# Kernel tuning notes

Measured on AMD Instinct MI355X. Metric: run time of the kernel, lower is better.

The kernel has to match this reference:

```python
import jax, jax.numpy as jnp
import numpy as np

BETA = 0.25  # commitment-loss weight (kwargs['beta'])


def setup_inputs() -> dict:
    key = jax.random.key(0)
    k1, k2 = jax.random.split(key)
    B, C, H, W = 16, 256, 64, 64
    K = 2048
    feats = jax.random.normal(k1, (B, C, H, W), dtype=jnp.float32)
    # nn.Embedding init: uniform(-1/n_codewords, 1/codeword_dim)
    codebook = jax.random.uniform(k2, (K, C), minval=-1.0 / K, maxval=1.0 / C,
                                  dtype=jnp.float32)
    return {"feats": feats, "codebook": codebook}


def reference(feats, codebook):
    B, C, H, W = feats.shape
    K = codebook.shape[0]
    z = jnp.transpose(feats, (0, 2, 3, 1))          # [B,H,W,C]
    zf = z.reshape(-1, C)                            # [N,C], N=B*H*W
    # squared-euclidean distances via ||z||^2 + ||e||^2 - 2 z.e : [N,K]
    d = (jnp.sum(zf * zf, axis=1, keepdims=True)
         + jnp.sum(codebook * codebook, axis=1)
         - 2.0 * (zf @ codebook.T))
    min_encoding_indices = jnp.argmin(d, axis=1)     # [N]
    mat_id_probs = jax.nn.softmax(-jnp.abs(d), axis=1)  # [N,K]
    z_q = codebook[min_encoding_indices].reshape(z.shape)  # [B,H,W,C]
    loss = (BETA * jnp.mean((jax.lax.stop_gradient(z_q) - z) ** 2)
            + jnp.mean((z_q - jax.lax.stop_gradient(z)) ** 2))
    # straight-through estimator
    z_q_st = z + jax.lax.stop_gradient(z_q - z)
    z_q_out = jnp.transpose(z_q_st, (0, 3, 1, 2))    # [B,C,H,W]
    idx_out = min_encoding_indices.reshape(B, H, W)
    probs_out = jnp.transpose(mat_id_probs.reshape(B, H, W, K), (0, 3, 1, 2))
    return z_q_out, idx_out, loss, probs_out
```

## Files before the change

kernel.cpp:

```cpp
#include <hip/hip_runtime.h>

#define HW 4096
#define CC 256
#define KK 2048
#define BB 16
#define NN (BB*HW)
#define RPB 128

#define ZQ_SZ   (BB*CC*HW)
#define IDX_OFF ZQ_SZ
#define LOSS_OFF (IDX_OFF + NN)
#define PROBS_OFF (LOSS_OFF + 1)

#define EH_OFF 0
#define EE_OFF 262144
#define EXT_OFF 264192
#define ZZ_OFF 280576

#define TAU 0.01f
#define CAND_CAP 512
#define KTC 32
#define KT_N 64
#define CS_N 17

typedef short bf16x8 __attribute__((ext_vector_type(8)));
typedef float f32x16 __attribute__((ext_vector_type(16)));
typedef unsigned int u32;

__device__ __forceinline__ void gload16(const void* g, void* l){
  __builtin_amdgcn_global_load_lds(
      (const __attribute__((address_space(1))) u32*)g,
      (__attribute__((address_space(3))) u32*)l, 16, 0, 0);
}

__device__ __forceinline__ unsigned short bf16rn(float x){
  unsigned u = __float_as_uint(x);
  return (unsigned short)((u + 0x7fffu + ((u >> 16) & 1u)) >> 16);
}

template<int STRIDE>
__device__ __forceinline__ float np_sumsq256(const float* __restrict__ a){
  float res0 = 0.f, res1 = 0.f;
  #pragma unroll
  for (int h = 0; h < 2; h++){
    const float* p = a + (size_t)h * 128 * STRIDE;
    float r[8];
    #pragma unroll
    for (int j = 0; j < 8; j++){ float x = p[(size_t)j * STRIDE]; r[j] = __fmul_rn(x, x); }
    for (int i = 8; i < 128; i += 8){
      #pragma unroll
      for (int j = 0; j < 8; j++){
        float x = p[(size_t)(i + j) * STRIDE];
        r[j] = __fadd_rn(r[j], __fmul_rn(x, x));
      }
    }
    float s = __fadd_rn(__fadd_rn(__fadd_rn(r[0], r[1]), __fadd_rn(r[2], r[3])),
                        __fadd_rn(__fadd_rn(r[4], r[5]), __fadd_rn(r[6], r[7])));
    if (h == 0) res0 = s; else res1 = s;
  }
  return __fadd_rn(res0, res1);
}

__global__ void k_prep2(const float* __restrict__ cb, float* __restrict__ out){
  const int k = blockIdx.x * 256 + threadIdx.x;
  unsigned short* eh = (unsigned short*)(out + EH_OFF);
  unsigned short* ex = (unsigned short*)(out + EXT_OFF);
  const float* row = cb + (size_t)k * CC;
  for (int c = 0; c < CC; c++) eh[k * CC + c] = bf16rn(row[c]);
  float ee = np_sumsq256<1>(row);
  out[EE_OFF + k] = ee;
  ex[k * 16] = bf16rn(-0.5f * ee);
  #pragma unroll
  for (int j = 1; j < 16; ++j) ex[k * 16 + j] = 0;
}

__global__ void k_zz(const float* __restrict__ feats, float* __restrict__ out){
  const int n = blockIdx.x * 256 + threadIdx.x;
  const int b = n >> 12, hw = n & 4095;
  out[ZZ_OFF + n] = np_sumsq256<HW>(feats + (size_t)b * CC * HW + hw);
}

__global__ __launch_bounds__(256, 4)
void k_mfma(const float* __restrict__ feats, const float* __restrict__ cb,
            float* __restrict__ out){
  __shared__ __align__(16) unsigned char lds_e[2][CS_N * 2 * KTC * 16];
  __shared__ unsigned long long rowkey[RPB];
  __shared__ int cand[CAND_CAP];
  __shared__ int cand_n;
  __shared__ float lsum;

  const int t = threadIdx.x;
  const int w = t >> 6, l = t & 63;
  const int grp = l >> 5;
  const int lane31 = l & 31;
  const int n0 = blockIdx.x * RPB;
  const int bi = n0 >> 12;
  const int hw0 = n0 & 4095;
  const int myhw = hw0 + w * 32 + lane31;

  if (t < RPB) rowkey[t] = ~0ull;
  if (t == 0){ cand_n = 0; lsum = 0.f; }

  bf16x8 ah0[16], ahx;
  {
    const float* zb = feats + (size_t)bi * CC * HW + myhw;
    #pragma unroll
    for (int cs = 0; cs < 16; ++cs){
      #pragma unroll
      for (int j = 0; j < 8; ++j)
        ah0[cs][j] = (short)bf16rn(zb[(size_t)(cs * 16 + grp * 8 + j) * HW]);
    }
    #pragma unroll
    for (int j = 0; j < 8; ++j) ahx[j] = 0;
    if (grp == 0) ahx[0] = (short)0x3F80;
  }

  const unsigned short* ehg = (const unsigned short*)(out + EH_OFF);
  const unsigned short* exg = (const unsigned short*)(out + EXT_OFF);

  int ofs_[4];
  #pragma unroll
  for (int i = 0; i < 4; ++i){
    int ix = i * 256 + t;
    int cd = ix & 31, g = (ix >> 5) & 1, cs = ix >> 6;
    ofs_[i] = cd * CC + cs * 16 + g * 8;
  }

#define STAGE(KT, B) { \
    const unsigned short* tb_ = ehg + (size_t)(KT) * (KTC * CC); \
    _Pragma("unroll") \
    for (int i_ = 0; i_ < 4; ++i_) \
      gload16(tb_ + ofs_[i_], &lds_e[B][(i_ * 256 + t) * 16]); \
    if (t < 64){ \
      int cd_ = t & 31, g_ = (t >> 5) & 1; \
      gload16(exg + ((size_t)((KT) * KTC + cd_) * 16 + g_ * 8), \
              &lds_e[B][(1024 + t) * 16]); \
    } }

#define COMPUTE(B) { \
    _Pragma("unroll") \
    for (int ii = 0; ii < 16; ++ii){ accA[ii] = 0.f; accB[ii] = 0.f; } \
    _Pragma("unroll") \
    for (int cs = 0; cs < 16; ++cs){ \
      const unsigned char* bp_ = &lds_e[B][(size_t)(cs * 2 + grp) * 512 + lane31 * 16]; \
      bf16x8 e_ = *(const bf16x8*)(bp_); \
      if (cs & 1) accB = __builtin_amdgcn_mfma_f32_32x32x16_bf16(e_, ah0[cs], accB, 0, 0, 0); \
      else        accA = __builtin_amdgcn_mfma_f32_32x32x16_bf16(e_, ah0[cs], accA, 0, 0, 0); \
    } \
    { \
      const unsigned char* bp_ = &lds_e[B][(size_t)(16 * 2 + grp) * 512 + lane31 * 16]; \
      bf16x8 e_ = *(const bf16x8*)(bp_); \
      accA = __builtin_amdgcn_mfma_f32_32x32x16_bf16(e_, ahx, accA, 0, 0, 0); \
    } }

  f32x16 accA, accB;
  float m0 = 3e38f, ss0 = 0.f, inv0 = 0.f;

  STAGE(0, 0);
  __syncthreads();

  for (int kt = 0; kt < 2 * KT_N; ++kt){
    const int tt = kt & 63;
    const int buf = kt & 1;
    if (kt < 2 * KT_N - 1) STAGE((kt + 1) & 63, buf ^ 1);
    COMPUTE(buf);
    if (kt < KT_N){
      #pragma unroll
      for (int r = 0; r < 16; ++r){
        float s = -2.f * (accA[r] + accB[r]);
        m0 = fminf(m0, s);
        ss0 += __expf(-s);
      }
      if (kt == KT_N - 1){
        m0 = fminf(m0, __shfl_xor(m0, 32));
        ss0 += __shfl_xor(ss0, 32);
        inv0 = 1.f / ss0;
      }
    } else {
      float* pb = out + (size_t)PROBS_OFF
                + (size_t)(bi * KK + tt * KTC + 4 * grp) * HW + myhw;
      #pragma unroll
      for (int r = 0; r < 16; ++r){
        int off = (r & 3) + 8 * (r >> 2);
        float s = -2.f * (accA[r] + accB[r]);
        pb[(size_t)off * HW] = __expf(-s) * inv0;
        if (s <= m0 + TAU){
          int sl = atomicAdd(&cand_n, 1);
          if (sl < CAND_CAP)
            cand[sl] = ((w * 32 + lane31) << 16) | (tt * KTC + 4 * grp + off);
        }
      }
    }
    __syncthreads();
  }

  int nc = cand_n; if (nc > CAND_CAP) nc = CAND_CAP;
  for (int i = t; i < nc; i += 256){
    int rc = cand[i];
    int rl = rc >> 16, code = rc & 0xffff;
    int n = n0 + rl;
    const float* zp = feats + (size_t)(n >> 12) * CC * HW + (n & 4095);
    const float* ep = cb + (size_t)code * CC;
    float a = 0.f;
    #pragma unroll 8
    for (int c = 0; c < CC; ++c) a = __builtin_fmaf(zp[(size_t)c * HW], ep[c], a);
    float t1 = __fadd_rn(out[ZZ_OFF + n], out[EE_OFF + code]);
    float d = __fadd_rn(t1, -2.f * a);
    unsigned long long key = ((unsigned long long)__float_as_uint(d) << 32) | (unsigned)code;
    atomicMin(&rowkey[rl], key);
  }
  __syncthreads();

  if (t < RPB) out[IDX_OFF + n0 + t] = (float)(int)(rowkey[t] & 0xffffffffu);

  if (t < RPB){
    int code = (int)(rowkey[t] & 0xffffffffu);
    const float* ep = cb + (size_t)code * CC;
    const float* zp = feats + (size_t)bi * CC * HW + hw0 + t;
    float s = 0.f;
    for (int c = 0; c < CC; ++c){
      float dz = ep[c] - zp[(size_t)c * HW];
      s = __builtin_fmaf(dz, dz, s);
    }
    atomicAdd(&lsum, s);
  }
  __syncthreads();
  if (t == 0) atomicAdd(out + LOSS_OFF, lsum * (1.25f / 16777216.f));
}

__global__ void k_zq(const float* __restrict__ cb, float* __restrict__ out){
  const int f4 = blockIdx.x * 256 + threadIdx.x;
  const int f = f4 * 4;
  const int b = f >> 20;
  const int rem = f & 1048575;
  const int c = rem >> 12;
  const int hw = rem & 4095;
  const int n = b * HW + hw;
  const float* idxf = out + IDX_OFF;
  float4 iv = *(const float4*)(idxf + n);
  float4 o;
  o.x = cb[(size_t)((int)iv.x) * CC + c];
  o.y = cb[(size_t)((int)iv.y) * CC + c];
  o.z = cb[(size_t)((int)iv.z) * CC + c];
  o.w = cb[(size_t)((int)iv.w) * CC + c];
  *(float4*)(out + f) = o;
}

extern "C" void kernel_launch(void* const* d_in, const int* in_sizes, int n_in,
                              void* d_out, int out_size, void* d_ws, size_t ws_size,
                              hipStream_t stream){
  const float* feats = (const float*)d_in[0];
  const float* cb    = (const float*)d_in[1];
  float* out = (float*)d_out;

  (void)hipMemsetAsync(out + LOSS_OFF, 0, sizeof(float), stream);
  hipLaunchKernelGGL(k_prep2, dim3(8),     dim3(256), 0, stream, cb, out);
  hipLaunchKernelGGL(k_zz,    dim3(256),   dim3(256), 0, stream, feats, out);
  hipLaunchKernelGGL(k_mfma,  dim3(512),   dim3(256), 0, stream, feats, cb, out);
  hipLaunchKernelGGL(k_zq,    dim3(16384), dim3(256), 0, stream, cb, out);
}
```

Measured before the change: 534.8 us.

## Split fused two-pass distance kernel into stats and probs kernels over codebook halves

Measured after the change: 534.4 us. Within noise of the previous version (-0.1%).

```diff
diff --git a/kernel.cpp b/kernel.cpp
--- a/kernel.cpp
+++ b/kernel.cpp
@@ -16,16 +16,20 @@
 #define EE_OFF 262144
 #define EXT_OFF 264192
 #define ZZ_OFF 280576
+#define MS_OFF 346112
+#define SS_OFF 477184
+#define IKEY_OFF 608256
 
 #define TAU 0.01f
 #define CAND_CAP 512
 #define KTC 32
-#define KT_N 64
+#define KT_N 32
 #define CS_N 17
 
 typedef short bf16x8 __attribute__((ext_vector_type(8)));
 typedef float f32x16 __attribute__((ext_vector_type(16)));
 typedef unsigned int u32;
+typedef unsigned long long u64;
 
 __device__ __forceinline__ void gload16(const void* g, void* l){
   __builtin_amdgcn_global_load_lds(
@@ -80,62 +84,50 @@
   out[ZZ_OFF + n] = np_sumsq256<HW>(feats + (size_t)b * CC * HW + hw);
 }
 
-__global__ __launch_bounds__(256, 4)
-void k_mfma(const float* __restrict__ feats, const float* __restrict__ cb,
-            float* __restrict__ out){
-  __shared__ __align__(16) unsigned char lds_e[2][CS_N * 2 * KTC * 16];
-  __shared__ unsigned long long rowkey[RPB];
-  __shared__ int cand[CAND_CAP];
-  __shared__ int cand_n;
-  __shared__ float lsum;
-
-  const int t = threadIdx.x;
-  const int w = t >> 6, l = t & 63;
-  const int grp = l >> 5;
-  const int lane31 = l & 31;
-  const int n0 = blockIdx.x * RPB;
-  const int bi = n0 >> 12;
-  const int hw0 = n0 & 4095;
-  const int myhw = hw0 + w * 32 + lane31;
-
-  if (t < RPB) rowkey[t] = ~0ull;
-  if (t == 0){ cand_n = 0; lsum = 0.f; }
-
-  bf16x8 ah0[16], ahx;
-  {
-    const float* zb = feats + (size_t)bi * CC * HW + myhw;
-    #pragma unroll
-    for (int cs = 0; cs < 16; ++cs){
-      #pragma unroll
-      for (int j = 0; j < 8; ++j)
-        ah0[cs][j] = (short)bf16rn(zb[(size_t)(cs * 16 + grp * 8 + j) * HW]);
-    }
-    #pragma unroll
-    for (int j = 0; j < 8; ++j) ahx[j] = 0;
-    if (grp == 0) ahx[0] = (short)0x3F80;
-  }
-
-  const unsigned short* ehg = (const unsigned short*)(out + EH_OFF);
-  const unsigned short* exg = (const unsigned short*)(out + EXT_OFF);
-
-  int ofs_[4];
-  #pragma unroll
-  for (int i = 0; i < 4; ++i){
-    int ix = i * 256 + t;
-    int cd = ix & 31, g = (ix >> 5) & 1, cs = ix >> 6;
-    ofs_[i] = cd * CC + cs * 16 + g * 8;
-  }
+
+#define GEMM_PROLOG \
+  const int t = threadIdx.x; \
+  const int w = t >> 6, l = t & 63; \
+  const int grp = l >> 5; \
+  const int lane31 = l & 31; \
+  const int bid = blockIdx.x; \
+  const int rb = bid >> 1, h = bid & 1; \
+  const int n0 = rb * RPB; \
+  const int bi = n0 >> 12; \
+  const int hw0 = n0 & 4095; \
+  const int myhw = hw0 + w * 32 + lane31; \
+  bf16x8 ah0[16], ahx; \
+  { \
+    const float* zb = feats + (size_t)bi * CC * HW + myhw; \
+    _Pragma("unroll") \
+    for (int cs = 0; cs < 16; ++cs){ \
+      _Pragma("unroll") \
+      for (int j = 0; j < 8; ++j) \
+        ah0[cs][j] = (short)bf16rn(zb[(size_t)(cs * 16 + grp * 8 + j) * HW]); \
+    } \
+    _Pragma("unroll") \
+    for (int j = 0; j < 8; ++j) ahx[j] = 0; \
+    if (grp == 0) ahx[0] = (short)0x3F80; \
+  } \
+  const unsigned short* ehg = (const unsigned short*)(out + EH_OFF) + (size_t)h * 1024 * CC; \
+  const unsigned short* exg = (const unsigned short*)(out + EXT_OFF) + (size_t)h * 1024 * 16; \
+  int ofs_[4]; \
+  _Pragma("unroll") \
+  for (int i = 0; i < 4; ++i){ \
+    int ix = i * 256 + t; \
+    int cd = ix & 31, g = (ix >> 5) & 1, cs = ix >> 6; \
+    ofs_[i] = cd * CC + cs * 16 + g * 8; \
+  } \
+  int x_ofs = 0; \
+  if (t < 64){ int cd = t & 31, g = (t >> 5) & 1; x_ofs = cd * 16 + g * 8; }
 
 #define STAGE(KT, B) { \
-    const unsigned short* tb_ = ehg + (size_t)(KT) * (KTC * CC); \
+    const size_t kto_ = (size_t)(KT) * (KTC * CC); \
     _Pragma("unroll") \
     for (int i_ = 0; i_ < 4; ++i_) \
-      gload16(tb_ + ofs_[i_], &lds_e[B][(i_ * 256 + t) * 16]); \
-    if (t < 64){ \
-      int cd_ = t & 31, g_ = (t >> 5) & 1; \
-      gload16(exg + ((size_t)((KT) * KTC + cd_) * 16 + g_ * 8), \
-              &lds_e[B][(1024 + t) * 16]); \
-    } }
+      gload16(ehg + ofs_[i_] + kto_, &lds_e[B][(i_ * 256 + t) * 16]); \
+    if (t < 64) \
+      gload16(exg + x_ofs + (size_t)(KT) * (KTC * 16), &lds_e[B][(1024 + t) * 16]); }
 
 #define COMPUTE(B) { \
     _Pragma("unroll") \
@@ -148,56 +140,86 @@
       else        accA = __builtin_amdgcn_mfma_f32_32x32x16_bf16(e_, ah0[cs], accA, 0, 0, 0); \
     } \
     { \
-      const unsigned char* bp_ = &lds_e[B][(size_t)(16 * 2 + grp) * 512 + lane31 * 16]; \
+      const unsigned char* bp_ = &lds_e[B][(size_t)(32 + grp) * 512 + lane31 * 16]; \
       bf16x8 e_ = *(const bf16x8*)(bp_); \
       accA = __builtin_amdgcn_mfma_f32_32x32x16_bf16(e_, ahx, accA, 0, 0, 0); \
     } }
 
+__global__ __launch_bounds__(256, 4)
+void k_stats(const float* __restrict__ feats, float* __restrict__ out){
+  __shared__ __align__(16) unsigned char lds_e[2][CS_N * 2 * KTC * 16];
+  GEMM_PROLOG
   f32x16 accA, accB;
-  float m0 = 3e38f, ss0 = 0.f, inv0 = 0.f;
+  float m0 = 3e38f, ss0 = 0.f;
 
   STAGE(0, 0);
   __syncthreads();
-
-  for (int kt = 0; kt < 2 * KT_N; ++kt){
-    const int tt = kt & 63;
+  for (int kt = 0; kt < KT_N; ++kt){
     const int buf = kt & 1;
-    if (kt < 2 * KT_N - 1) STAGE((kt + 1) & 63, buf ^ 1);
+    if (kt < KT_N - 1) STAGE(kt + 1, buf ^ 1);
     COMPUTE(buf);
-    if (kt < KT_N){
-      #pragma unroll
-      for (int r = 0; r < 16; ++r){
-        float s = -2.f * (accA[r] + accB[r]);
-        m0 = fminf(m0, s);
-        ss0 += __expf(-s);
-      }
-      if (kt == KT_N - 1){
-        m0 = fminf(m0, __shfl_xor(m0, 32));
-        ss0 += __shfl_xor(ss0, 32);
-        inv0 = 1.f / ss0;
-      }
-    } else {
-      float* pb = out + (size_t)PROBS_OFF
-                + (size_t)(bi * KK + tt * KTC + 4 * grp) * HW + myhw;
-      #pragma unroll
-      for (int r = 0; r < 16; ++r){
-        int off = (r & 3) + 8 * (r >> 2);
-        float s = -2.f * (accA[r] + accB[r]);
-        pb[(size_t)off * HW] = __expf(-s) * inv0;
-        if (s <= m0 + TAU){
-          int sl = atomicAdd(&cand_n, 1);
-          if (sl < CAND_CAP)
-            cand[sl] = ((w * 32 + lane31) << 16) | (tt * KTC + 4 * grp + off);
-        }
+    #pragma unroll
+    for (int r = 0; r < 16; ++r){
+      float s = -2.f * (accA[r] + accB[r]);
+      m0 = fminf(m0, s);
+      ss0 += __expf(-s);
+    }
+    __syncthreads();
+  }
+  m0 = fminf(m0, __shfl_xor(m0, 32));
+  ss0 += __shfl_xor(ss0, 32);
+  if (grp == 0){
+    out[MS_OFF + h * NN + n0 + w * 32 + lane31] = m0;
+    out[SS_OFF + h * NN + n0 + w * 32 + lane31] = ss0;
+  }
+}
+
+__global__ __launch_bounds__(256, 4)
+void k_probs(const float* __restrict__ feats, const float* __restrict__ cb,
+             float* __restrict__ out){
+  __shared__ __align__(16) unsigned char lds_e[2][CS_N * 2 * KTC * 16];
+  __shared__ int cand[CAND_CAP];
+  __shared__ int cand_n;
+  GEMM_PROLOG
+  if (t == 0) cand_n = 0;
+  f32x16 accA, accB;
+
+  const int myrow = n0 + w * 32 + lane31;
+  float m0, inv0;
+  {
+    float ma = out[MS_OFF + myrow], mb = out[MS_OFF + NN + myrow];
+    float sa = out[SS_OFF + myrow], sb = out[SS_OFF + NN + myrow];
+    m0 = fminf(ma, mb);
+    inv0 = 1.f / (sa + sb);
+  }
+
+  STAGE(0, 0);
+  __syncthreads();
+  for (int kt = 0; kt < KT_N; ++kt){
+    const int buf = kt & 1;
+    if (kt < KT_N - 1) STAGE(kt + 1, buf ^ 1);
+    COMPUTE(buf);
+    float* pb = out + (size_t)PROBS_OFF
+              + (size_t)(bi * KK + h * 1024 + kt * KTC + 4 * grp) * HW + myhw;
+    #pragma unroll
+    for (int r = 0; r < 16; ++r){
+      int off = (r & 3) + 8 * (r >> 2);
+      float s = -2.f * (accA[r] + accB[r]);
+      pb[(size_t)off * HW] = __expf(-s) * inv0;
+      if (s <= m0 + TAU){
+        int sl = atomicAdd(&cand_n, 1);
+        if (sl < CAND_CAP)
+          cand[sl] = ((w * 32 + lane31) << 16) | (h * 1024 + kt * KTC + 4 * grp + off);
       }
     }
     __syncthreads();
   }
 
+  u64* ikey = (u64*)(out + IKEY_OFF);
   int nc = cand_n; if (nc > CAND_CAP) nc = CAND_CAP;
   for (int i = t; i < nc; i += 256){
     int rc = cand[i];
-    int rl = rc >> 16, code = rc & 0xffff;
+    int rl = (rc >> 16) & 127, code = rc & 2047;
     int n = n0 + rl;
     const float* zp = feats + (size_t)(n >> 12) * CC * HW + (n & 4095);
     const float* ep = cb + (size_t)code * CC;
@@ -206,26 +228,29 @@
     for (int c = 0; c < CC; ++c) a = __builtin_fmaf(zp[(size_t)c * HW], ep[c], a);
     float t1 = __fadd_rn(out[ZZ_OFF + n], out[EE_OFF + code]);
     float d = __fadd_rn(t1, -2.f * a);
-    unsigned long long key = ((unsigned long long)__float_as_uint(d) << 32) | (unsigned)code;
-    atomicMin(&rowkey[rl], key);
-  }
-  __syncthreads();
-
-  if (t < RPB) out[IDX_OFF + n0 + t] = (float)(int)(rowkey[t] & 0xffffffffu);
-
-  if (t < RPB){
-    int code = (int)(rowkey[t] & 0xffffffffu);
-    const float* ep = cb + (size_t)code * CC;
-    const float* zp = feats + (size_t)bi * CC * HW + hw0 + t;
-    float s = 0.f;
-    for (int c = 0; c < CC; ++c){
-      float dz = ep[c] - zp[(size_t)c * HW];
-      s = __builtin_fmaf(dz, dz, s);
-    }
-    atomicAdd(&lsum, s);
-  }
-  __syncthreads();
-  if (t == 0) atomicAdd(out + LOSS_OFF, lsum * (1.25f / 16777216.f));
+    u64 key = ((u64)__float_as_uint(d) << 32) | (unsigned)code;
+    atomicMin(&ikey[n], key);
+  }
+}
+
+__global__ void k_final(const float* __restrict__ feats, const float* __restrict__ cb,
+                        float* __restrict__ out){
+  const int t = threadIdx.x;
+  const int n = blockIdx.x * 256 + t;
+  const u64* ikey = (const u64*)(out + IKEY_OFF);
+  int code = (int)(ikey[n] & 2047u);
+  out[IDX_OFF + n] = (float)code;
+  const int bi = n >> 12, hw = n & 4095;
+  const float* ep = cb + (size_t)code * CC;
+  const float* zp = feats + (size_t)bi * CC * HW + hw;
+  float s = 0.f;
+  for (int c = 0; c < CC; ++c){
+    float dz = ep[c] - zp[(size_t)c * HW];
+    s = __builtin_fmaf(dz, dz, s);
+  }
+  #pragma unroll
+  for (int off = 32; off; off >>= 1) s += __shfl_xor(s, off);
+  if ((t & 63) == 0) atomicAdd(out + LOSS_OFF, s * (1.25f / 16777216.f));
 }
 
 __global__ void k_zq(const float* __restrict__ cb, float* __restrict__ out){
@@ -254,8 +279,11 @@
   float* out = (float*)d_out;
 
   (void)hipMemsetAsync(out + LOSS_OFF, 0, sizeof(float), stream);
+  (void)hipMemsetAsync(out + IKEY_OFF, 0xFF, (size_t)NN * 8, stream);
   hipLaunchKernelGGL(k_prep2, dim3(8),     dim3(256), 0, stream, cb, out);
   hipLaunchKernelGGL(k_zz,    dim3(256),   dim3(256), 0, stream, feats, out);
-  hipLaunchKernelGGL(k_mfma,  dim3(512),   dim3(256), 0, stream, feats, cb, out);
+  hipLaunchKernelGGL(k_stats, dim3(1024),  dim3(256), 0, stream, feats, out);
+  hipLaunchKernelGGL(k_probs, dim3(1024),  dim3(256), 0, stream, feats, cb, out);
+  hipLaunchKernelGGL(k_final, dim3(256),   dim3(256), 0, stream, feats, cb, out);
   hipLaunchKernelGGL(k_zq,    dim3(16384), dim3(256), 0, stream, cb, out);
 }
```
